# Kernel optimization log

Measured on AMD Instinct MI355X. Metric: run time of the kernel, lower is better.

Reference implementation:

```python
import jax, jax.numpy as jnp
import numpy as np

N = 50000        # nodes
E = 800000       # edges
R = 8            # relations
G = 64           # g_dim
H1 = 64          # h1_dim
H2 = 32          # h2_dim (per-head for transformer, output for sage)
HEADS = 4
EPS = 1e-5       # BatchNorm eps


def setup_inputs() -> dict:
    key = jax.random.key(0)
    ks = jax.random.split(key, 16)
    def rn(k, shape, scale=0.05):
        return jax.random.normal(k, shape, dtype=jnp.float32) * scale
    return {
        "node_features": jax.random.normal(ks[0], (N, G), dtype=jnp.float32),
        "node_type": jax.random.randint(ks[1], (N,), 0, 3),
        "edge_index": jax.random.randint(ks[2], (2, E), 0, N),
        "edge_type": jax.random.randint(ks[3], (E,), 0, R),
        # RGCNConv params (per-relation weight + root weight + bias)
        "rgcn_w": rn(ks[4], (R, G, H1)),
        "rgcn_root": rn(ks[5], (G, H1)),
        "rgcn_bias": jnp.zeros((H1,), jnp.float32),
        "bn1_g": jnp.ones((H1,), jnp.float32),
        "bn1_b": jnp.zeros((H1,), jnp.float32),
        # TransformerConv params (q/k/v projections + skip)
        "wq": rn(ks[6], (H1, HEADS * H2)), "bq": jnp.zeros((HEADS * H2,), jnp.float32),
        "wk": rn(ks[7], (H1, HEADS * H2)), "bk": jnp.zeros((HEADS * H2,), jnp.float32),
        "wv": rn(ks[8], (H1, HEADS * H2)), "bv": jnp.zeros((HEADS * H2,), jnp.float32),
        "wskip": rn(ks[9], (H1, HEADS * H2)), "bskip": jnp.zeros((HEADS * H2,), jnp.float32),
        "bn2_g": jnp.ones((HEADS * H2,), jnp.float32),
        "bn2_b": jnp.zeros((HEADS * H2,), jnp.float32),
        # SAGEConv params (lin_l on aggregated neighbors has bias; lin_r on root has none)
        "sage_wl": rn(ks[10], (HEADS * H2, H2)), "sage_bl": jnp.zeros((H2,), jnp.float32),
        "sage_wr": rn(ks[11], (HEADS * H2, H2)),
        "bn3_g": jnp.ones((H2,), jnp.float32),
        "bn3_b": jnp.zeros((H2,), jnp.float32),
    }


def _bn(x, g, b):
    # BatchNorm1d in training mode: biased batch statistics over nodes
    m = x.mean(0)
    v = x.var(0)
    return g * (x - m) * jax.lax.rsqrt(v + EPS) + b


def _match(res, d):
    # F.pad(res, (0, d - c)): pads with zeros if d > c, truncates if d < c
    c = res.shape[1]
    if d > c:
        return jnp.pad(res, ((0, 0), (0, d - c)))
    return res[:, :d]


def _forward(node_features, rgcn_w, rgcn_root, rgcn_bias, bn1_g, bn1_b,
             wq, bq, wk, bk, wv, bv, wskip, bskip, bn2_g, bn2_b,
             sage_wl, sage_bl, sage_wr, bn3_g, bn3_b,
             edge_index, edge_type):
    src, dst = edge_index[0], edge_index[1]
    x = node_features
    residual = x

    # ---- RGCNConv: per-relation transform, per-relation mean aggregation, sum over relations ----
    xr = jnp.einsum('nf,rfh->nrh', x, rgcn_w)            # [N,R,H1]
    msg = xr[src, edge_type]                              # [E,H1]
    seg = dst * R + edge_type                             # segment per (node, relation)
    sums = jax.ops.segment_sum(msg, seg, num_segments=N * R)
    cnt = jax.ops.segment_sum(jnp.ones((E,), msg.dtype), seg, num_segments=N * R)
    agg = (sums / jnp.maximum(cnt, 1.0)[:, None]).reshape(N, R, H1).sum(1)
    h = agg + x @ rgcn_root + rgcn_bias
    h = jax.nn.leaky_relu(_bn(h, bn1_g, bn1_b))
    x = h + _match(residual, h.shape[1])
    residual = x

    # ---- TransformerConv: edge softmax attention, concat heads, + skip projection ----
    q = (x @ wq + bq).reshape(N, HEADS, H2)
    k = (x @ wk + bk).reshape(N, HEADS, H2)
    v = (x @ wv + bv).reshape(N, HEADS, H2)
    logits = (q[dst] * k[src]).sum(-1) / jnp.sqrt(jnp.float32(H2))  # [E,HEADS]
    mx = jax.ops.segment_max(logits, dst, num_segments=N)
    ex = jnp.exp(logits - mx[dst])
    den = jax.ops.segment_sum(ex, dst, num_segments=N)
    alpha = ex / jnp.maximum(den[dst], 1e-16)
    out = jax.ops.segment_sum(alpha[:, :, None] * v[src], dst, num_segments=N)
    h = out.reshape(N, HEADS * H2) + x @ wskip + bskip
    h = jax.nn.leaky_relu(_bn(h, bn2_g, bn2_b))
    x = h + _match(residual, h.shape[1])
    residual = x

    # ---- SAGEConv: mean neighbor aggregation + root transform ----
    nsum = jax.ops.segment_sum(x[src], dst, num_segments=N)
    ncnt = jax.ops.segment_sum(jnp.ones((E,), x.dtype), dst, num_segments=N)
    nmean = nsum / jnp.maximum(ncnt, 1.0)[:, None]
    h = nmean @ sage_wl + sage_bl + x @ sage_wr
    h = jax.nn.leaky_relu(_bn(h, bn3_g, bn3_b))
    return h + _match(residual, h.shape[1])


def reference(node_features, node_type, edge_index, edge_type,
              rgcn_w, rgcn_root, rgcn_bias, bn1_g, bn1_b,
              wq, bq, wk, bk, wv, bv, wskip, bskip, bn2_g, bn2_b,
              sage_wl, sage_bl, sage_wr, bn3_g, bn3_b):
    # node_type is unused by the original forward
    return _forward(node_features, rgcn_w, rgcn_root, rgcn_bias, bn1_g, bn1_b,
                    wq, bq, wk, bk, wv, bv, wskip, bskip, bn2_g, bn2_b,
                    sage_wl, sage_bl, sage_wr, bn3_g, bn3_b,
                    edge_index, edge_type)
```

## Files before the change

### kernel.cpp

```cpp
#include <hip/hip_runtime.h>
#include <stdint.h>

#define NN 50000
#define NE 800000
#define NR (NN*8)
#define SCAN_BS 512
#define NB2 782
#define INV_N (1.0f/50000.0f)
#define BN_EPS 1e-5f

typedef unsigned short ushort_t;
typedef unsigned char uchar_t;
typedef short bf16x8 __attribute__((ext_vector_type(8)));
typedef float f32x4 __attribute__((ext_vector_type(4)));
typedef float f32x2 __attribute__((ext_vector_type(2)));

__device__ __forceinline__ ushort_t f2bf(float f){
    unsigned int u = __float_as_uint(f);
    u += 0x7FFFu + ((u >> 16) & 1u);
    return (ushort_t)(u >> 16);
}
__device__ __forceinline__ float bf2f(ushort_t h){ return __uint_as_float(((unsigned int)h) << 16); }
__device__ __forceinline__ float bflo(unsigned int u){ return __uint_as_float(u << 16); }
__device__ __forceinline__ float bfhi(unsigned int u){ return __uint_as_float(u & 0xFFFF0000u); }

__device__ __forceinline__ unsigned int f4_to_fp8(float a, float b, float c, float d){
    int v = __builtin_amdgcn_cvt_pk_fp8_f32(a, b, 0, false);
    v = __builtin_amdgcn_cvt_pk_fp8_f32(c, d, v, true);
    return (unsigned int)v;
}
__device__ __forceinline__ void fp8_to_f4(unsigned int u, float& a, float& b, float& c, float& d){
    f32x2 lo = __builtin_amdgcn_cvt_pk_f32_fp8(u, false);
    f32x2 hi = __builtin_amdgcn_cvt_pk_f32_fp8(u, true);
    a = lo.x; b = lo.y; c = hi.x; d = hi.y;
}

__global__ void k_prep(const float* __restrict__ nf,
                       const float* __restrict__ rgcn_w, const float* __restrict__ root,
                       const float* __restrict__ wq, const float* __restrict__ wk,
                       const float* __restrict__ wv, const float* __restrict__ wsk,
                       const float* __restrict__ bq, const float* __restrict__ bk,
                       const float* __restrict__ bv, const float* __restrict__ bsk,
                       const float* __restrict__ wl, const float* __restrict__ wr,
                       const int* __restrict__ ei, const int* __restrict__ et,
                       int* __restrict__ deg, uint2* __restrict__ sr,
                       ushort_t* __restrict__ xb, uchar_t* __restrict__ xb8,
                       ushort_t* __restrict__ Wcat,
                       ushort_t* __restrict__ Wt2, float* __restrict__ bcat,
                       ushort_t* __restrict__ Wsage){
    int i = blockIdx.x*256 + threadIdx.x;
    const int NXB = NN*16;
    if (i < NXB){
        float4 v = ((const float4*)nf)[i];
        ushort4 h;
        h.x = f2bf(v.x); h.y = f2bf(v.y); h.z = f2bf(v.z); h.w = f2bf(v.w);
        ((ushort4*)xb)[i] = h;
        ((unsigned int*)xb8)[i] = f4_to_fp8(v.x, v.y, v.z, v.w);
        return;
    }
    int j = i - NXB;
    if (j < 64*576){
        int h = j / 576, k = j - h*576;
        float v = (k < 512) ? rgcn_w[(size_t)k*64 + h] : root[(size_t)(k-512)*64 + h];
        Wcat[j] = f2bf(v);
    } else if (j < 64*576 + 512*64){
        int jj = j - 64*576;
        int c = jj >> 6, k = jj & 63;
        int mt = c >> 7, cc = c & 127;
        const float* W = (mt==0)?wq:(mt==1)?wk:(mt==2)?wv:wsk;
        Wt2[jj] = f2bf(W[(size_t)k*128 + cc]);
    } else if (j < 64*576 + 512*64 + 512){
        int c = j - (64*576 + 512*64);
        int mt = c >> 7, cc = c & 127;
        const float* B = (mt==0)?bq:(mt==1)?bk:(mt==2)?bv:bsk;
        bcat[c] = B[cc];
    } else if (j < 64*576 + 512*64 + 512 + 32*256){
        int jj = j - (64*576 + 512*64 + 512);
        int c = jj >> 8, k = jj & 255;
        float v = (k < 128) ? wr[(size_t)k*32 + c] : wl[(size_t)(k-128)*32 + c];
        Wsage[jj] = f2bf(v);
    } else {
        int e = j - (64*576 + 512*64 + 512 + 32*256);
        if (e < NE){
            int seg = ei[NE + e]*8 + et[e];
            int rank = atomicAdd(&deg[seg], 1);
            uint2 o; o.x = (unsigned)seg; o.y = (unsigned)rank;
            sr[e] = o;
        }
    }
}

__global__ void k_scan1(const int* __restrict__ deg, int* __restrict__ tmp, int* __restrict__ bsum){
    __shared__ int s[SCAN_BS];
    int t = threadIdx.x;
    int i = blockIdx.x*SCAN_BS + t;
    s[t] = (i < NR) ? deg[i] : 0;
    __syncthreads();
    for (int off = 1; off < SCAN_BS; off <<= 1){
        int add = (t >= off) ? s[t-off] : 0;
        __syncthreads();
        s[t] += add;
        __syncthreads();
    }
    if (i < NR) tmp[i] = s[t];
    if (t == SCAN_BS-1) bsum[blockIdx.x] = s[t];
}

__global__ void k_scan2(int* __restrict__ bsum){
    __shared__ int s[1024];
    int t = threadIdx.x;
    s[t] = (t < NB2) ? bsum[t] : 0;
    __syncthreads();
    for (int off = 1; off < 1024; off <<= 1){
        int v = (t >= off) ? s[t-off] : 0;
        __syncthreads();
        s[t] += v;
        __syncthreads();
    }
    if (t < NB2) bsum[t] = s[t];
}

__global__ void k_scan3(const int* __restrict__ tmp, const int* __restrict__ bsum, int* __restrict__ rs){
    int i = blockIdx.x*256 + threadIdx.x;
    if (i < NR){
        int b = i >> 9;
        int off = (b > 0) ? bsum[b-1] : 0;
        rs[i+1] = tmp[i] + off;
        if (i == 0) rs[0] = 0;
    }
}

__global__ void k_fill(const int* __restrict__ ei, const uint2* __restrict__ sr,
                       const int* __restrict__ rs, int* __restrict__ csr){
    int e = blockIdx.x*256 + threadIdx.x;
    if (e < NE){
        uint2 s = sr[e];
        csr[rs[s.x] + (int)s.y] = ei[e];
    }
}

__global__ __launch_bounds__(256) void rgcn_fused(const ushort_t* __restrict__ xb,
                                                  const uchar_t* __restrict__ xb8,
                                                  const int* __restrict__ rs,
                                                  const int* __restrict__ csr,
                                                  const ushort_t* __restrict__ Wcat,
                                                  const float* __restrict__ bias,
                                                  float* __restrict__ h1pre){
    __shared__ ushort_t Ml[16*520];
    int w = threadIdx.x >> 6, lane = threadIdx.x & 63;
    int quad = lane >> 4, l4 = lane & 15;
    int row0 = blockIdx.x * 16;
    int n0 = row0 + w*4;
    int rsel = (lane < 9 ? lane : 8);
    int rb = rs[n0*8 + rsel];
    int eb0 = __shfl(rb, 0);
    int dg0 = __shfl(rb, 8) - eb0;
    int idx = (lane < dg0) ? csr[eb0 + lane] : 0;
    for (int j = 0; j < 4; ++j){
        int lrow = (w*4 + j)*520;
        int ebase = __shfl(rb, 0);
        int enext = __shfl(rb, 8);
        int rb_next = 0, idxn = 0;
        if (j < 3){
            rb_next = rs[(n0 + j + 1)*8 + rsel];
            idxn = csr[min(enext + lane, NE - 1)];
        }
        int e0a = __shfl(rb, quad),     e1a = __shfl(rb, quad + 1);
        int e0b = __shfl(rb, quad + 4), e1b = __shfl(rb, quad + 5);
        int oa = e0a - ebase, la = e1a - e0a;
        int ob = e0b - ebase, lb = e1b - e0b;
        int laf = min(la, max(64 - oa, 0));
        int lbf = min(lb, max(64 - ob, 0));
        int ml = max(laf, lbf);
        ml = max(ml, __shfl_xor(ml, 16));
        ml = max(ml, __shfl_xor(ml, 32));
        f32x2 aA0 = {0.f,0.f}, aA1 = {0.f,0.f};
        f32x2 aB0 = {0.f,0.f}, aB1 = {0.f,0.f};
        for (int i = 0; i < ml; i += 4){
            unsigned int uA[4], uB[4];
#pragma unroll
            for (int u = 0; u < 4; ++u){
                int jA = oa + i + u, jB = ob + i + u;
                int tA = __shfl(idx, jA & 63);
                int tB = __shfl(idx, jB & 63);
                tA = ((i + u) < laf) ? tA : 0;
                tB = ((i + u) < lbf) ? tB : 0;
                uA[u] = *(const unsigned int*)(xb8 + (size_t)tA*64 + l4*4);
                uB[u] = *(const unsigned int*)(xb8 + (size_t)tB*64 + l4*4);
            }
#pragma unroll
            for (int u = 0; u < 4; ++u){
                unsigned int a = ((i + u) < laf) ? uA[u] : 0u;
                unsigned int b = ((i + u) < lbf) ? uB[u] : 0u;
                aA0 += __builtin_amdgcn_cvt_pk_f32_fp8(a, false);
                aA1 += __builtin_amdgcn_cvt_pk_f32_fp8(a, true);
                aB0 += __builtin_amdgcn_cvt_pk_f32_fp8(b, false);
                aB1 += __builtin_amdgcn_cvt_pk_f32_fp8(b, true);
            }
        }
        for (int i = laf; i < la; ++i){
            int t = csr[e0a + i];
            unsigned int a = *(const unsigned int*)(xb8 + (size_t)t*64 + l4*4);
            aA0 += __builtin_amdgcn_cvt_pk_f32_fp8(a, false);
            aA1 += __builtin_amdgcn_cvt_pk_f32_fp8(a, true);
        }
        for (int i = lbf; i < lb; ++i){
            int t = csr[e0b + i];
            unsigned int b = *(const unsigned int*)(xb8 + (size_t)t*64 + l4*4);
            aB0 += __builtin_amdgcn_cvt_pk_f32_fp8(b, false);
            aB1 += __builtin_amdgcn_cvt_pk_f32_fp8(b, true);
        }
        float inva = 1.f / fmaxf((float)la, 1.f);
        float invb = 1.f / fmaxf((float)lb, 1.f);
        ushort4 oA, oB;
        oA.x = f2bf(aA0.x*inva); oA.y = f2bf(aA0.y*inva); oA.z = f2bf(aA1.x*inva); oA.w = f2bf(aA1.y*inva);
        oB.x = f2bf(aB0.x*invb); oB.y = f2bf(aB0.y*invb); oB.z = f2bf(aB1.x*invb); oB.w = f2bf(aB1.y*invb);
        *(ushort4*)&Ml[lrow + quad*64 + l4*4] = oA;
        *(ushort4*)&Ml[lrow + (quad + 4)*64 + l4*4] = oB;
        if (j < 3){
            rb = rb_next;
            int ebn = __shfl(rb, 0);
            int dgn = __shfl(rb, 8) - ebn;
            idx = (lane < dgn) ? idxn : 0;
        }
    }
    __syncthreads();
    int m = l4;
    f32x4 acc = {};
#pragma unroll
    for (int kt = 0; kt < 18; ++kt){
        int kk = kt*32 + quad*8;
        bf16x8 a;
        if (kt < 16) a = *(const bf16x8*)&Ml[m*520 + kk];
        else         a = *(const bf16x8*)(xb + (size_t)(row0 + m)*64 + (kk - 512));
        bf16x8 b = *(const bf16x8*)(Wcat + (size_t)(w*16 + m)*576 + kk);
        acc = __builtin_amdgcn_mfma_f32_16x16x32_bf16(a, b, acc, 0, 0, 0);
    }
    int col = w*16 + m;
    float bz = bias[col];
#pragma unroll
    for (int i = 0; i < 4; ++i){
        int rr = row0 + quad*4 + i;
        h1pre[(size_t)rr*64 + col] = acc[i] + bz;
    }
}

#define QS 132
#define BS 68
__global__ __launch_bounds__(256) void gemm_qkvs(const float* __restrict__ h1pre,
                                                 const float* __restrict__ nf,
                                                 const float* __restrict__ s1, const float* __restrict__ q1,
                                                 const float* __restrict__ g1, const float* __restrict__ b1,
                                                 const ushort_t* __restrict__ Wt2,
                                                 const float* __restrict__ bcat,
                                                 ushort_t* __restrict__ qb,
                                                 uchar_t* __restrict__ kb8,
                                                 uchar_t* __restrict__ vb8,
                                                 ushort_t* __restrict__ sb){
    __shared__ ushort_t Bs[256*BS];
    __shared__ ushort_t pl[4][16*QS];
    int w = threadIdx.x >> 6, lane = threadIdx.x & 63;
    int m = lane & 15, quad = lane >> 4;
    int r0 = blockIdx.x*64 + w*16;
    int cg = blockIdx.y;
    int row = r0 + m;
    {
        int t = threadIdx.x;
        const ushort_t* wsrc = Wt2 + (size_t)cg*256*64;
#pragma unroll
        for (int u0 = 0; u0 < 8; ++u0){
            int u = u0*256 + t;
            int r = u >> 3, c8 = (u & 7)*8;
            *(uint4*)&Bs[r*BS + c8] = *(const uint4*)(wsrc + u*8);
        }
    }
    bf16x8 afrag[2];
#pragma unroll
    for (int kt = 0; kt < 2; ++kt){
        int db = kt*32 + quad*8;
        bf16x8 f = (bf16x8){0,0,0,0,0,0,0,0};
        if (row < NN){
            float4 h0 = *(const float4*)(h1pre + (size_t)row*64 + db);
            float4 h1 = *(const float4*)(h1pre + (size_t)row*64 + db + 4);
            float4 n0 = *(const float4*)(nf + (size_t)row*64 + db);
            float4 n1 = *(const float4*)(nf + (size_t)row*64 + db + 4);
            float4 sa = *(const float4*)(s1 + db);
            float4 sb_ = *(const float4*)(s1 + db + 4);
            float4 qa = *(const float4*)(q1 + db);
            float4 qb_ = *(const float4*)(q1 + db + 4);
            float4 ga = *(const float4*)(g1 + db);
            float4 gb_ = *(const float4*)(g1 + db + 4);
            float4 ba = *(const float4*)(b1 + db);
            float4 bb_ = *(const float4*)(b1 + db + 4);
            float hh[8] = {h0.x,h0.y,h0.z,h0.w,h1.x,h1.y,h1.z,h1.w};
            float nn[8] = {n0.x,n0.y,n0.z,n0.w,n1.x,n1.y,n1.z,n1.w};
            float SS[8] = {sa.x,sa.y,sa.z,sa.w,sb_.x,sb_.y,sb_.z,sb_.w};
            float QQ[8] = {qa.x,qa.y,qa.z,qa.w,qb_.x,qb_.y,qb_.z,qb_.w};
            float GG[8] = {ga.x,ga.y,ga.z,ga.w,gb_.x,gb_.y,gb_.z,gb_.w};
            float BB[8] = {ba.x,ba.y,ba.z,ba.w,bb_.x,bb_.y,bb_.z,bb_.w};
#pragma unroll
            for (int e = 0; e < 8; ++e){
                float mm = SS[e] * INV_N;
                float vv = QQ[e] * INV_N - mm*mm;
                float A = rsqrtf(fmaxf(vv, 0.f) + BN_EPS) * GG[e];
                float C = BB[e] - mm * A;
                float y = fmaf(hh[e], A, C);
                y = (y >= 0.f) ? y : 0.01f*y;
                f[e] = (short)f2bf(y + nn[e]);
            }
        }
        afrag[kt] = f;
    }
    __syncthreads();
    f32x4 acc[16] = {};
#pragma unroll
    for (int kt = 0; kt < 2; ++kt){
        int kk = kt*32 + quad*8;
#pragma unroll
        for (int ct = 0; ct < 16; ++ct){
            bf16x8 b = *(const bf16x8*)&Bs[(size_t)(ct*16 + m)*BS + kk];
            acc[ct] = __builtin_amdgcn_mfma_f32_16x16x32_bf16(afrag[kt], b, acc[ct], 0, 0, 0);
        }
    }
#pragma unroll
    for (int ct = 0; ct < 8; ++ct){
        int g = cg*256 + ct*16 + m;
        float bz = bcat[g];
        int cc = g & 127;
#pragma unroll
        for (int i = 0; i < 4; ++i)
            pl[w][(quad*4 + i)*QS + cc] = f2bf(acc[ct][i] + bz);
    }
    if (cg == 0){
#pragma unroll
        for (int t = 0; t < 4; ++t){
            int u = t*64 + lane;
            int r = u >> 4, c = (u & 15)*8;
            int gr = r0 + r;
            if (gr < NN) *(uint4*)(qb + (size_t)gr*128 + c) = *(const uint4*)&pl[w][r*QS + c];
        }
    } else {
#pragma unroll
        for (int t = 0; t < 4; ++t){
            int u = t*64 + lane;
            int r = u >> 4, c = (u & 15)*8;
            int gr = r0 + r;
            if (gr < NN){
                uint4 vv4 = *(const uint4*)&pl[w][r*QS + c];
                uint2 o;
                o.x = f4_to_fp8(bflo(vv4.x), bfhi(vv4.x), bflo(vv4.y), bfhi(vv4.y));
                o.y = f4_to_fp8(bflo(vv4.z), bfhi(vv4.z), bflo(vv4.w), bfhi(vv4.w));
                *(uint2*)(vb8 + (size_t)gr*128 + c) = o;
            }
        }
    }
#pragma unroll
    for (int ct = 8; ct < 16; ++ct){
        int g = cg*256 + ct*16 + m;
        float bz = bcat[g];
        int cc = g & 127;
#pragma unroll
        for (int i = 0; i < 4; ++i)
            pl[w][(quad*4 + i)*QS + cc] = f2bf(acc[ct][i] + bz);
    }
    if (cg == 0){
#pragma unroll
        for (int t = 0; t < 4; ++t){
            int u = t*64 + lane;
            int r = u >> 4, c = (u & 15)*8;
            int gr = r0 + r;
            if (gr < NN){
                uint4 kk4 = *(const uint4*)&pl[w][r*QS + c];
                uint2 o;
                o.x = f4_to_fp8(bflo(kk4.x), bfhi(kk4.x), bflo(kk4.y), bfhi(kk4.y));
                o.y = f4_to_fp8(bflo(kk4.z), bfhi(kk4.z), bflo(kk4.w), bfhi(kk4.w));
                *(uint2*)(kb8 + (size_t)gr*128 + c) = o;
            }
        }
    } else {
#pragma unroll
        for (int t = 0; t < 4; ++t){
            int u = t*64 + lane;
            int r = u >> 4, c = (u & 15)*8;
            int gr = r0 + r;
            if (gr < NN) *(uint4*)(sb + (size_t)gr*128 + c) = *(const uint4*)&pl[w][r*QS + c];
        }
    }
}

__global__ __launch_bounds__(256) void sage_gemm(const ushort_t* __restrict__ x2b,
                                                 const ushort_t* __restrict__ nmeanb,
                                                 const ushort_t* __restrict__ Wsage,
                                                 const float* __restrict__ bl,
                                                 float* __restrict__ h3){
    int wv = threadIdx.x >> 6, lane = threadIdx.x & 63;
    int r0 = blockIdx.x*64 + wv*16;
    int m = lane & 15, quad = lane >> 4;
    int row = r0 + m;
    f32x4 acc[2] = {};
#pragma unroll
    for (int kt = 0; kt < 8; ++kt){
        int kk = kt*32 + quad*8;
        bf16x8 a;
        if (row < NN){
            const ushort_t* ap = (kt < 4) ? (x2b + (size_t)row*128 + kk)
                                          : (nmeanb + (size_t)row*128 + (kk - 128));
            a = *(const bf16x8*)ap;
        } else {
            a = (bf16x8){0,0,0,0,0,0,0,0};
        }
#pragma unroll
        for (int ct = 0; ct < 2; ++ct){
            bf16x8 b = *(const bf16x8*)(Wsage + (size_t)(ct*16 + m)*256 + kk);
            acc[ct] = __builtin_amdgcn_mfma_f32_16x16x32_bf16(a, b, acc[ct], 0, 0, 0);
        }
    }
#pragma unroll
    for (int ct = 0; ct < 2; ++ct){
        int col = ct*16 + m;
        float bz = bl[col];
#pragma unroll
        for (int i = 0; i < 4; ++i){
            int rr = r0 + quad*4 + i;
            if (rr < NN) h3[(size_t)rr*32 + col] = acc[ct][i] + bz;
        }
    }
}

template<int C>
__global__ __launch_bounds__(256) void bn_stats(const float* __restrict__ X, int ld,
                                                float* __restrict__ sums, float* __restrict__ sumsq){
    __shared__ float s1[256], s2[256];
    int t = threadIdx.x;
    int c = t & (C-1);
    const int rpb = 256 / C;
    int r = blockIdx.x * rpb + (t / C);
    int rstride = gridDim.x * rpb;
    float a = 0.f, b = 0.f;
    for (; r < NN; r += rstride){
        float v = X[(size_t)r*ld + c];
        a += v; b += v*v;
    }
    s1[t] = a; s2[t] = b;
    __syncthreads();
    for (int off = 128; off >= C; off >>= 1){
        if (t < off){ s1[t] += s1[t+off]; s2[t] += s2[t+off]; }
        __syncthreads();
    }
    if (t < C){ atomicAdd(&sums[t], s1[t]); atomicAdd(&sumsq[t], s2[t]); }
}

__device__ __forceinline__ float bn_leaky(float z, float m, float rsv, float g, float b){
    float y = (z - m) * rsv * g + b;
    return y >= 0.f ? y : 0.01f * y;
}

__global__ void bn_apply2(const float* __restrict__ h2, const float* __restrict__ h1pre,
                          const float* __restrict__ nf,
                          const float* __restrict__ g1, const float* __restrict__ b1,
                          const float* __restrict__ s1, const float* __restrict__ q1,
                          const float* __restrict__ g2, const float* __restrict__ b2,
                          const float* __restrict__ s2, const float* __restrict__ q2,
                          float* __restrict__ x2r, ushort_t* __restrict__ x2b,
                          uchar_t* __restrict__ x28){
    int i = blockIdx.x*256 + threadIdx.x;
    if (i >= NN*128) return;
    int n = i >> 7, c = i & 127;
    float m2 = s2[c] * INV_N;
    float v2 = q2[c] * INV_N - m2*m2;
    float rsv2 = rsqrtf(fmaxf(v2, 0.f) + BN_EPS);
    float val = bn_leaky(h2[i], m2, rsv2, g2[c], b2[c]);
    if (c < 64){
        float m1 = s1[c] * INV_N;
        float v1 = q1[c] * INV_N - m1*m1;
        float rsv1 = rsqrtf(fmaxf(v1, 0.f) + BN_EPS);
        val += bn_leaky(h1pre[(size_t)n*64 + c], m1, rsv1, g1[c], b1[c]) + nf[(size_t)n*64 + c];
    }
    if (c < 32) x2r[(size_t)n*32 + c] = val;
    x2b[i] = f2bf(val);
    int p = __builtin_amdgcn_cvt_pk_fp8_f32(val, val, 0, false);
    x28[i] = (uchar_t)(p & 0xFF);
}

__global__ void bn_apply3(const float* __restrict__ h3, const float* __restrict__ x2r,
                          const float* __restrict__ g, const float* __restrict__ b,
                          const float* __restrict__ sums, const float* __restrict__ sumsq,
                          float* __restrict__ out){
    int i = blockIdx.x*256 + threadIdx.x;
    if (i >= NN*32) return;
    int c = i & 31;
    float m = sums[c] * INV_N;
    float v = sumsq[c] * INV_N - m*m;
    float rsv = rsqrtf(fmaxf(v, 0.f) + BN_EPS);
    out[i] = bn_leaky(h3[i], m, rsv, g[c], b[c]) + x2r[i];
}

__global__ __launch_bounds__(256) void attn_kernel(const ushort_t* __restrict__ qb,
                                                   const uchar_t* __restrict__ kb8,
                                                   const uchar_t* __restrict__ vb8,
                                                   const ushort_t* __restrict__ sb,
                                                   const int* __restrict__ rs,
                                                   const int* __restrict__ csr,
                                                   float* __restrict__ h2){
    int w = threadIdx.x >> 6, lane = threadIdx.x & 63;
    int n = blockIdx.x*4 + w;
    if (n >= NN) return;
    int half = lane >> 5, l5 = lane & 31;
    int e0 = rs[n*8], e1 = rs[n*8 + 8];
    int deg = e1 - e0;
    uint2 qu = *(const uint2*)(qb + (size_t)n*128 + l5*4);
    uint2 sbv = *(const uint2*)(sb + (size_t)n*128 + l5*4);
    float q0 = bflo(qu.x), q1 = bfhi(qu.x), q2 = bflo(qu.y), q3 = bfhi(qu.y);
    const float scale = 0.17677669529663687f;
    int idx = 0;
    if (lane < deg) idx = csr[e0 + lane];
    int dcap = min(deg, 64);
    int nt = (dcap + 7) >> 3;
    float den = 0.f, a0 = 0.f, a1 = 0.f, a2 = 0.f, a3 = 0.f;
    for (int t = 0; t < nt; ++t){
        int i2 = t*8 + half*4;
        int j0 = i2, j1 = i2+1, j2 = i2+2, j3 = i2+3;
        bool v0 = j0 < dcap, v1 = j1 < dcap, v2 = j2 < dcap, v3 = j3 < dcap;
        int s0 = __shfl(idx, j0 & 63); s0 = v0 ? s0 : 0;
        int s1 = __shfl(idx, j1 & 63); s1 = v1 ? s1 : 0;
        int s2 = __shfl(idx, j2 & 63); s2 = v2 ? s2 : 0;
        int s3 = __shfl(idx, j3 & 63); s3 = v3 ? s3 : 0;
        unsigned int ku0 = *(const unsigned int*)(kb8 + (size_t)s0*128 + l5*4);
        unsigned int ku1 = *(const unsigned int*)(kb8 + (size_t)s1*128 + l5*4);
        unsigned int ku2 = *(const unsigned int*)(kb8 + (size_t)s2*128 + l5*4);
        unsigned int ku3 = *(const unsigned int*)(kb8 + (size_t)s3*128 + l5*4);
        unsigned int vu0 = *(const unsigned int*)(vb8 + (size_t)s0*128 + l5*4);
        unsigned int vu1 = *(const unsigned int*)(vb8 + (size_t)s1*128 + l5*4);
        unsigned int vu2 = *(const unsigned int*)(vb8 + (size_t)s2*128 + l5*4);
        unsigned int vu3 = *(const unsigned int*)(vb8 + (size_t)s3*128 + l5*4);
        float ka, kb_, kc, kd;
        fp8_to_f4(ku0, ka, kb_, kc, kd);
        float p0 = q0*ka + q1*kb_ + q2*kc + q3*kd;
        fp8_to_f4(ku1, ka, kb_, kc, kd);
        float p1 = q0*ka + q1*kb_ + q2*kc + q3*kd;
        fp8_to_f4(ku2, ka, kb_, kc, kd);
        float p2 = q0*ka + q1*kb_ + q2*kc + q3*kd;
        fp8_to_f4(ku3, ka, kb_, kc, kd);
        float p3 = q0*ka + q1*kb_ + q2*kc + q3*kd;
        p0 += __shfl_xor(p0, 1); p1 += __shfl_xor(p1, 1); p2 += __shfl_xor(p2, 1); p3 += __shfl_xor(p3, 1);
        p0 += __shfl_xor(p0, 2); p1 += __shfl_xor(p1, 2); p2 += __shfl_xor(p2, 2); p3 += __shfl_xor(p3, 2);
        p0 += __shfl_xor(p0, 4); p1 += __shfl_xor(p1, 4); p2 += __shfl_xor(p2, 4); p3 += __shfl_xor(p3, 4);
        float w0 = v0 ? __expf(p0 * scale) : 0.f;
        float w1 = v1 ? __expf(p1 * scale) : 0.f;
        float w2 = v2 ? __expf(p2 * scale) : 0.f;
        float w3 = v3 ? __expf(p3 * scale) : 0.f;
        den += w0 + w1 + w2 + w3;
        float va, vb_, vc, vd;
        fp8_to_f4(vu0, va, vb_, vc, vd);
        a0 = fmaf(w0, va, a0); a1 = fmaf(w0, vb_, a1); a2 = fmaf(w0, vc, a2); a3 = fmaf(w0, vd, a3);
        fp8_to_f4(vu1, va, vb_, vc, vd);
        a0 = fmaf(w1, va, a0); a1 = fmaf(w1, vb_, a1); a2 = fmaf(w1, vc, a2); a3 = fmaf(w1, vd, a3);
        fp8_to_f4(vu2, va, vb_, vc, vd);
        a0 = fmaf(w2, va, a0); a1 = fmaf(w2, vb_, a1); a2 = fmaf(w2, vc, a2); a3 = fmaf(w2, vd, a3);
        fp8_to_f4(vu3, va, vb_, vc, vd);
        a0 = fmaf(w3, va, a0); a1 = fmaf(w3, vb_, a1); a2 = fmaf(w3, vc, a2); a3 = fmaf(w3, vd, a3);
    }
    for (int e = 64 + half; e < deg; e += 2){
        int s = csr[e0 + e];
        unsigned int ku = *(const unsigned int*)(kb8 + (size_t)s*128 + l5*4);
        unsigned int vu = *(const unsigned int*)(vb8 + (size_t)s*128 + l5*4);
        float ka, kb_, kc, kd;
        fp8_to_f4(ku, ka, kb_, kc, kd);
        float p = q0*ka + q1*kb_ + q2*kc + q3*kd;
        p += __shfl_xor(p, 1);
        p += __shfl_xor(p, 2);
        p += __shfl_xor(p, 4);
        float wg = __expf(p * scale);
        den += wg;
        float va, vb_, vc, vd;
        fp8_to_f4(vu, va, vb_, vc, vd);
        a0 = fmaf(wg, va, a0); a1 = fmaf(wg, vb_, a1); a2 = fmaf(wg, vc, a2); a3 = fmaf(wg, vd, a3);
    }
    den += __shfl_xor(den, 32);
    a0 += __shfl_xor(a0, 32); a1 += __shfl_xor(a1, 32);
    a2 += __shfl_xor(a2, 32); a3 += __shfl_xor(a3, 32);
    if (half == 0){
        float inv = (den > 0.f) ? 1.f/den : 0.f;
        float4 o;
        o.x = bflo(sbv.x) + a0*inv;
        o.y = bfhi(sbv.x) + a1*inv;
        o.z = bflo(sbv.y) + a2*inv;
        o.w = bfhi(sbv.y) + a3*inv;
        *(float4*)(h2 + (size_t)n*128 + l5*4) = o;
    }
}

__global__ __launch_bounds__(256) void sage_agg(const uchar_t* __restrict__ x28,
                                                const int* __restrict__ rs,
                                                const int* __restrict__ csr,
                                                ushort_t* __restrict__ nmeanb){
    int w = threadIdx.x >> 6, lane = threadIdx.x & 63;
    int n = blockIdx.x*4 + w;
    if (n >= NN) return;
    int half = lane >> 5, l5 = lane & 31;
    int e0 = rs[n*8], e1 = rs[n*8 + 8];
    int deg = e1 - e0;
    int idx = 0;
    if (lane < deg) idx = csr[e0 + lane];
    int dcap = min(deg, 64);
    int nt = (dcap + 7) >> 3;
    f32x2 A0 = {0.f,0.f}, A1 = {0.f,0.f};
    for (int t = 0; t < nt; ++t){
        int i2 = t*8 + half*4;
        int j0 = i2, j1 = i2+1, j2 = i2+2, j3 = i2+3;
        bool v0 = j0 < dcap, v1 = j1 < dcap, v2 = j2 < dcap, v3 = j3 < dcap;
        int s0 = __shfl(idx, j0 & 63); s0 = v0 ? s0 : 0;
        int s1 = __shfl(idx, j1 & 63); s1 = v1 ? s1 : 0;
        int s2 = __shfl(idx, j2 & 63); s2 = v2 ? s2 : 0;
        int s3 = __shfl(idx, j3 & 63); s3 = v3 ? s3 : 0;
        unsigned int u0 = *(const unsigned int*)(x28 + (size_t)s0*128 + l5*4);
        unsigned int u1 = *(const unsigned int*)(x28 + (size_t)s1*128 + l5*4);
        unsigned int u2 = *(const unsigned int*)(x28 + (size_t)s2*128 + l5*4);
        unsigned int u3 = *(const unsigned int*)(x28 + (size_t)s3*128 + l5*4);
        u0 = v0 ? u0 : 0u; u1 = v1 ? u1 : 0u;
        u2 = v2 ? u2 : 0u; u3 = v3 ? u3 : 0u;
        A0 += __builtin_amdgcn_cvt_pk_f32_fp8(u0, false);
        A1 += __builtin_amdgcn_cvt_pk_f32_fp8(u0, true);
        A0 += __builtin_amdgcn_cvt_pk_f32_fp8(u1, false);
        A1 += __builtin_amdgcn_cvt_pk_f32_fp8(u1, true);
        A0 += __builtin_amdgcn_cvt_pk_f32_fp8(u2, false);
        A1 += __builtin_amdgcn_cvt_pk_f32_fp8(u2, true);
        A0 += __builtin_amdgcn_cvt_pk_f32_fp8(u3, false);
        A1 += __builtin_amdgcn_cvt_pk_f32_fp8(u3, true);
    }
    for (int e = 64 + half; e < deg; e += 2){
        int s = csr[e0 + e];
        unsigned int u = *(const unsigned int*)(x28 + (size_t)s*128 + l5*4);
        A0 += __builtin_amdgcn_cvt_pk_f32_fp8(u, false);
        A1 += __builtin_amdgcn_cvt_pk_f32_fp8(u, true);
    }
    float a0 = A0.x, a1 = A0.y, a2 = A1.x, a3 = A1.y;
    a0 += __shfl_xor(a0, 32); a1 += __shfl_xor(a1, 32);
    a2 += __shfl_xor(a2, 32); a3 += __shfl_xor(a3, 32);
    if (half == 0){
        float inv = 1.f / fmaxf((float)deg, 1.f);
        ushort4 o;
        o.x = f2bf(a0*inv); o.y = f2bf(a1*inv); o.z = f2bf(a2*inv); o.w = f2bf(a3*inv);
        *(ushort4*)(nmeanb + (size_t)n*128 + l5*4) = o;
    }
}

extern "C" void kernel_launch(void* const* d_in, const int* in_sizes, int n_in,
                              void* d_out, int out_size, void* d_ws, size_t ws_size,
                              hipStream_t stream){
    const float* nf      = (const float*)d_in[0];
    const int*   ei      = (const int*)d_in[2];
    const int*   et      = (const int*)d_in[3];
    const float* rgcn_w  = (const float*)d_in[4];
    const float* root    = (const float*)d_in[5];
    const float* rbias   = (const float*)d_in[6];
    const float* bn1g    = (const float*)d_in[7];
    const float* bn1b    = (const float*)d_in[8];
    const float* wq      = (const float*)d_in[9];
    const float* bq      = (const float*)d_in[10];
    const float* wk      = (const float*)d_in[11];
    const float* bk      = (const float*)d_in[12];
    const float* wv      = (const float*)d_in[13];
    const float* bv      = (const float*)d_in[14];
    const float* wsk     = (const float*)d_in[15];
    const float* bsk     = (const float*)d_in[16];
    const float* bn2g    = (const float*)d_in[17];
    const float* bn2b    = (const float*)d_in[18];
    const float* wl      = (const float*)d_in[19];
    const float* bl      = (const float*)d_in[20];
    const float* wr      = (const float*)d_in[21];
    const float* bn3g    = (const float*)d_in[22];
    const float* bn3b    = (const float*)d_in[23];
    float* out = (float*)d_out;

    char* base = (char*)d_ws;
    size_t off = 0;
    auto take = [&](size_t bytes) -> char* {
        char* p = base + off;
        off += (bytes + 255) & ~(size_t)255;
        return p;
    };
    int*      deg    = (int*)take((size_t)NR*4);
    float*    bns    = (float*)take(1024*4);
    char*     zend   = base + off;
    int*      rs     = (int*)take((size_t)(NR+1)*4);
    int*      tmp    = (int*)take((size_t)NR*4);
    int*      bsum   = (int*)take(1024*4);
    uint2*    sr     = (uint2*)take((size_t)NE*8);
    int*      csr    = (int*)take((size_t)NE*4);
    ushort_t* Wcat   = (ushort_t*)take(64*576*2);
    ushort_t* Wt2    = (ushort_t*)take(512*64*2);
    float*    bcat   = (float*)take(512*4);
    ushort_t* Wsage  = (ushort_t*)take(32*256*2);
    ushort_t* xb     = (ushort_t*)take((size_t)NN*64*2);
    uchar_t*  xb8    = (uchar_t*)take((size_t)NN*64);
    float*    h1pre  = (float*)take((size_t)NN*64*4);
    float*    h2     = (float*)take((size_t)NN*128*4);
    float*    x2r    = (float*)take((size_t)NN*32*4);
    ushort_t* sb     = (ushort_t*)take((size_t)NN*128*2);
    char*     bigA   = take((size_t)NN*512*2);
    if (off > ws_size) return;

    ushort_t* qb     = (ushort_t*)(bigA + (size_t)NN*128);
    uchar_t*  vb8    = (uchar_t*)(bigA + (size_t)NN*384);
    uchar_t*  kb8    = (uchar_t*)(bigA + (size_t)NN*640);
    ushort_t* x2b    = (ushort_t*)bigA;
    uchar_t*  x28    = (uchar_t*)(bigA + (size_t)NN*256);
    ushort_t* nmeanb = (ushort_t*)(bigA + (size_t)NN*512);
    float*    h3     = (float*)(bigA + (size_t)NN*768);

    hipMemsetAsync(deg, 0, (size_t)(zend - (char*)deg), stream);

    const int PREP_N = NN*16 + 64*576 + 512*64 + 512 + 32*256 + NE;
    k_prep <<<(PREP_N+255)/256, 256, 0, stream>>>(nf, rgcn_w, root, wq, wk, wv, wsk,
                                                  bq, bk, bv, bsk, wl, wr,
                                                  ei, et, deg, sr,
                                                  xb, xb8, Wcat, Wt2, bcat, Wsage);
    k_scan1<<<NB2, SCAN_BS, 0, stream>>>(deg, tmp, bsum);
    k_scan2<<<1, 1024, 0, stream>>>(bsum);
    k_scan3<<<(NR+255)/256, 256, 0, stream>>>(tmp, bsum, rs);
    k_fill <<<(NE+255)/256, 256, 0, stream>>>(ei, sr, rs, csr);

    const int NB4 = (NN + 3) / 4;
    const int NBG = (NN + 63) / 64;

    rgcn_fused<<<NN/16, 256, 0, stream>>>(xb, xb8, rs, csr, Wcat, rbias, h1pre);
    bn_stats<64><<<256, 256, 0, stream>>>(h1pre, 64, bns + 0, bns + 64);

    gemm_qkvs<<<dim3(NBG, 2), 256, 0, stream>>>(h1pre, nf, bns + 0, bns + 64, bn1g, bn1b,
                                                Wt2, bcat, qb, kb8, vb8, sb);
    attn_kernel<<<NB4, 256, 0, stream>>>(qb, kb8, vb8, sb, rs, csr, h2);
    bn_stats<128><<<256, 256, 0, stream>>>(h2, 128, bns + 128, bns + 256);
    bn_apply2<<<(NN*128+255)/256, 256, 0, stream>>>(h2, h1pre, nf,
                                                    bn1g, bn1b, bns + 0, bns + 64,
                                                    bn2g, bn2b, bns + 128, bns + 256,
                                                    x2r, x2b, x28);

    sage_agg<<<NB4, 256, 0, stream>>>(x28, rs, csr, nmeanb);
    sage_gemm<<<NBG, 256, 0, stream>>>(x2b, nmeanb, Wsage, bl, h3);
    bn_stats<32><<<256, 256, 0, stream>>>(h3, 32, bns + 384, bns + 416);
    bn_apply3<<<(NN*32+255)/256, 256, 0, stream>>>(h3, x2r, bn3g, bn3b, bns + 384, bns + 416, out);
}
```

Baseline: 401.7 us.

## Fuse BatchNorm statistics into producer kernels and merge QKV column groups

```diff
diff --git a/kernel.cpp b/kernel.cpp
--- a/kernel.cpp
+++ b/kernel.cpp
@@ -145,7 +145,8 @@
                                                   const int* __restrict__ csr,
                                                   const ushort_t* __restrict__ Wcat,
                                                   const float* __restrict__ bias,
-                                                  float* __restrict__ h1pre){
+                                                  float* __restrict__ h1pre,
+                                                  float* __restrict__ bns){
     __shared__ ushort_t Ml[16*520];
     int w = threadIdx.x >> 6, lane = threadIdx.x & 63;
     int quad = lane >> 4, l4 = lane & 15;
@@ -238,10 +239,19 @@
     }
     int col = w*16 + m;
     float bz = bias[col];
+    float s = 0.f, q = 0.f;
 #pragma unroll
     for (int i = 0; i < 4; ++i){
         int rr = row0 + quad*4 + i;
-        h1pre[(size_t)rr*64 + col] = acc[i] + bz;
+        float y = acc[i] + bz;
+        h1pre[(size_t)rr*64 + col] = y;
+        s += y; q += y*y;
+    }
+    s += __shfl_xor(s, 16); q += __shfl_xor(q, 16);
+    s += __shfl_xor(s, 32); q += __shfl_xor(q, 32);
+    if (quad == 0){
+        atomicAdd(&bns[col], s);
+        atomicAdd(&bns[64 + col], q);
     }
 }
 
@@ -262,18 +272,7 @@
     int w = threadIdx.x >> 6, lane = threadIdx.x & 63;
     int m = lane & 15, quad = lane >> 4;
     int r0 = blockIdx.x*64 + w*16;
-    int cg = blockIdx.y;
     int row = r0 + m;
-    {
-        int t = threadIdx.x;
-        const ushort_t* wsrc = Wt2 + (size_t)cg*256*64;
-#pragma unroll
-        for (int u0 = 0; u0 < 8; ++u0){
-            int u = u0*256 + t;
-            int r = u >> 3, c8 = (u & 7)*8;
-            *(uint4*)&Bs[r*BS + c8] = *(const uint4*)(wsrc + u*8);
-        }
-    }
     bf16x8 afrag[2];
 #pragma unroll
     for (int kt = 0; kt < 2; ++kt){
@@ -311,79 +310,92 @@
         }
         afrag[kt] = f;
     }
-    __syncthreads();
-    f32x4 acc[16] = {};
-#pragma unroll
-    for (int kt = 0; kt < 2; ++kt){
-        int kk = kt*32 + quad*8;
-#pragma unroll
-        for (int ct = 0; ct < 16; ++ct){
-            bf16x8 b = *(const bf16x8*)&Bs[(size_t)(ct*16 + m)*BS + kk];
-            acc[ct] = __builtin_amdgcn_mfma_f32_16x16x32_bf16(afrag[kt], b, acc[ct], 0, 0, 0);
-        }
-    }
-#pragma unroll
-    for (int ct = 0; ct < 8; ++ct){
-        int g = cg*256 + ct*16 + m;
-        float bz = bcat[g];
-        int cc = g & 127;
-#pragma unroll
-        for (int i = 0; i < 4; ++i)
-            pl[w][(quad*4 + i)*QS + cc] = f2bf(acc[ct][i] + bz);
-    }
-    if (cg == 0){
-#pragma unroll
-        for (int t = 0; t < 4; ++t){
-            int u = t*64 + lane;
-            int r = u >> 4, c = (u & 15)*8;
-            int gr = r0 + r;
-            if (gr < NN) *(uint4*)(qb + (size_t)gr*128 + c) = *(const uint4*)&pl[w][r*QS + c];
-        }
-    } else {
-#pragma unroll
-        for (int t = 0; t < 4; ++t){
-            int u = t*64 + lane;
-            int r = u >> 4, c = (u & 15)*8;
-            int gr = r0 + r;
-            if (gr < NN){
-                uint4 vv4 = *(const uint4*)&pl[w][r*QS + c];
-                uint2 o;
-                o.x = f4_to_fp8(bflo(vv4.x), bfhi(vv4.x), bflo(vv4.y), bfhi(vv4.y));
-                o.y = f4_to_fp8(bflo(vv4.z), bfhi(vv4.z), bflo(vv4.w), bfhi(vv4.w));
-                *(uint2*)(vb8 + (size_t)gr*128 + c) = o;
-            }
-        }
-    }
-#pragma unroll
-    for (int ct = 8; ct < 16; ++ct){
-        int g = cg*256 + ct*16 + m;
-        float bz = bcat[g];
-        int cc = g & 127;
-#pragma unroll
-        for (int i = 0; i < 4; ++i)
-            pl[w][(quad*4 + i)*QS + cc] = f2bf(acc[ct][i] + bz);
-    }
-    if (cg == 0){
-#pragma unroll
-        for (int t = 0; t < 4; ++t){
-            int u = t*64 + lane;
-            int r = u >> 4, c = (u & 15)*8;
-            int gr = r0 + r;
-            if (gr < NN){
-                uint4 kk4 = *(const uint4*)&pl[w][r*QS + c];
-                uint2 o;
-                o.x = f4_to_fp8(bflo(kk4.x), bfhi(kk4.x), bflo(kk4.y), bfhi(kk4.y));
-                o.y = f4_to_fp8(bflo(kk4.z), bfhi(kk4.z), bflo(kk4.w), bfhi(kk4.w));
-                *(uint2*)(kb8 + (size_t)gr*128 + c) = o;
-            }
-        }
-    } else {
-#pragma unroll
-        for (int t = 0; t < 4; ++t){
-            int u = t*64 + lane;
-            int r = u >> 4, c = (u & 15)*8;
-            int gr = r0 + r;
-            if (gr < NN) *(uint4*)(sb + (size_t)gr*128 + c) = *(const uint4*)&pl[w][r*QS + c];
+    for (int cg = 0; cg < 2; ++cg){
+        __syncthreads();
+        {
+            int t = threadIdx.x;
+            const ushort_t* wsrc = Wt2 + (size_t)cg*256*64;
+#pragma unroll
+            for (int u0 = 0; u0 < 8; ++u0){
+                int u = u0*256 + t;
+                int r = u >> 3, c8 = (u & 7)*8;
+                *(uint4*)&Bs[r*BS + c8] = *(const uint4*)(wsrc + u*8);
+            }
+        }
+        __syncthreads();
+        f32x4 acc[16] = {};
+#pragma unroll
+        for (int kt = 0; kt < 2; ++kt){
+            int kk = kt*32 + quad*8;
+#pragma unroll
+            for (int ct = 0; ct < 16; ++ct){
+                bf16x8 b = *(const bf16x8*)&Bs[(size_t)(ct*16 + m)*BS + kk];
+                acc[ct] = __builtin_amdgcn_mfma_f32_16x16x32_bf16(afrag[kt], b, acc[ct], 0, 0, 0);
+            }
+        }
+#pragma unroll
+        for (int ct = 0; ct < 8; ++ct){
+            int g = cg*256 + ct*16 + m;
+            float bz = bcat[g];
+            int cc = g & 127;
+#pragma unroll
+            for (int i = 0; i < 4; ++i)
+                pl[w][(quad*4 + i)*QS + cc] = f2bf(acc[ct][i] + bz);
+        }
+        if (cg == 0){
+#pragma unroll
+            for (int t = 0; t < 4; ++t){
+                int u = t*64 + lane;
+                int r = u >> 4, c = (u & 15)*8;
+                int gr = r0 + r;
+                if (gr < NN) *(uint4*)(qb + (size_t)gr*128 + c) = *(const uint4*)&pl[w][r*QS + c];
+            }
+        } else {
+#pragma unroll
+            for (int t = 0; t < 4; ++t){
+                int u = t*64 + lane;
+                int r = u >> 4, c = (u & 15)*8;
+                int gr = r0 + r;
+                if (gr < NN){
+                    uint4 vv4 = *(const uint4*)&pl[w][r*QS + c];
+                    uint2 o;
+                    o.x = f4_to_fp8(bflo(vv4.x), bfhi(vv4.x), bflo(vv4.y), bfhi(vv4.y));
+                    o.y = f4_to_fp8(bflo(vv4.z), bfhi(vv4.z), bflo(vv4.w), bfhi(vv4.w));
+                    *(uint2*)(vb8 + (size_t)gr*128 + c) = o;
+                }
+            }
+        }
+#pragma unroll
+        for (int ct = 8; ct < 16; ++ct){
+            int g = cg*256 + ct*16 + m;
+            float bz = bcat[g];
+            int cc = g & 127;
+#pragma unroll
+            for (int i = 0; i < 4; ++i)
+                pl[w][(quad*4 + i)*QS + cc] = f2bf(acc[ct][i] + bz);
+        }
+        if (cg == 0){
+#pragma unroll
+            for (int t = 0; t < 4; ++t){
+                int u = t*64 + lane;
+                int r = u >> 4, c = (u & 15)*8;
+                int gr = r0 + r;
+                if (gr < NN){
+                    uint4 kk4 = *(const uint4*)&pl[w][r*QS + c];
+                    uint2 o;
+                    o.x = f4_to_fp8(bflo(kk4.x), bfhi(kk4.x), bflo(kk4.y), bfhi(kk4.y));
+                    o.y = f4_to_fp8(bflo(kk4.z), bfhi(kk4.z), bflo(kk4.w), bfhi(kk4.w));
+                    *(uint2*)(kb8 + (size_t)gr*128 + c) = o;
+                }
+            }
+        } else {
+#pragma unroll
+            for (int t = 0; t < 4; ++t){
+                int u = t*64 + lane;
+                int r = u >> 4, c = (u & 15)*8;
+                int gr = r0 + r;
+                if (gr < NN) *(uint4*)(sb + (size_t)gr*128 + c) = *(const uint4*)&pl[w][r*QS + c];
+            }
         }
     }
 }
@@ -392,7 +404,8 @@
                                                  const ushort_t* __restrict__ nmeanb,
                                                  const ushort_t* __restrict__ Wsage,
                                                  const float* __restrict__ bl,
-                                                 float* __restrict__ h3){
+                                                 float* __restrict__ h3,
+                                                 float* __restrict__ bns3){
     int wv = threadIdx.x >> 6, lane = threadIdx.x & 63;
     int r0 = blockIdx.x*64 + wv*16;
     int m = lane & 15, quad = lane >> 4;
@@ -415,6 +428,7 @@
             acc[ct] = __builtin_amdgcn_mfma_f32_16x16x32_bf16(a, b, acc[ct], 0, 0, 0);
         }
     }
+    float s[2] = {0.f, 0.f}, q[2] = {0.f, 0.f};
 #pragma unroll
     for (int ct = 0; ct < 2; ++ct){
         int col = ct*16 + m;
@@ -422,32 +436,26 @@
 #pragma unroll
         for (int i = 0; i < 4; ++i){
             int rr = r0 + quad*4 + i;
-            if (rr < NN) h3[(size_t)rr*32 + col] = acc[ct][i] + bz;
-        }
-    }
-}
-
-template<int C>
-__global__ __launch_bounds__(256) void bn_stats(const float* __restrict__ X, int ld,
-                                                float* __restrict__ sums, float* __restrict__ sumsq){
-    __shared__ float s1[256], s2[256];
-    int t = threadIdx.x;
-    int c = t & (C-1);
-    const int rpb = 256 / C;
-    int r = blockIdx.x * rpb + (t / C);
-    int rstride = gridDim.x * rpb;
-    float a = 0.f, b = 0.f;
-    for (; r < NN; r += rstride){
-        float v = X[(size_t)r*ld + c];
-        a += v; b += v*v;
-    }
-    s1[t] = a; s2[t] = b;
-    __syncthreads();
-    for (int off = 128; off >= C; off >>= 1){
-        if (t < off){ s1[t] += s1[t+off]; s2[t] += s2[t+off]; }
-        __syncthreads();
-    }
-    if (t < C){ atomicAdd(&sums[t], s1[t]); atomicAdd(&sumsq[t], s2[t]); }
+            if (rr < NN){
+                float y = acc[ct][i] + bz;
+                h3[(size_t)rr*32 + col] = y;
+                s[ct] += y; q[ct] += y*y;
+            }
+        }
+    }
+#pragma unroll
+    for (int ct = 0; ct < 2; ++ct){
+        s[ct] += __shfl_xor(s[ct], 16); q[ct] += __shfl_xor(q[ct], 16);
+        s[ct] += __shfl_xor(s[ct], 32); q[ct] += __shfl_xor(q[ct], 32);
+    }
+    if (quad == 0){
+#pragma unroll
+        for (int ct = 0; ct < 2; ++ct){
+            int col = ct*16 + m;
+            atomicAdd(&bns3[col], s[ct]);
+            atomicAdd(&bns3[32 + col], q[ct]);
+        }
+    }
 }
 
 __device__ __forceinline__ float bn_leaky(float z, float m, float rsv, float g, float b){
@@ -501,10 +509,11 @@
                                                    const ushort_t* __restrict__ sb,
                                                    const int* __restrict__ rs,
                                                    const int* __restrict__ csr,
-                                                   float* __restrict__ h2){
+                                                   float* __restrict__ h2,
+                                                   float* __restrict__ bns2){
+    __shared__ float sm[2][4][128];
     int w = threadIdx.x >> 6, lane = threadIdx.x & 63;
     int n = blockIdx.x*4 + w;
-    if (n >= NN) return;
     int half = lane >> 5, l5 = lane & 31;
     int e0 = rs[n*8], e1 = rs[n*8 + 8];
     int deg = e1 - e0;
@@ -579,14 +588,26 @@
     den += __shfl_xor(den, 32);
     a0 += __shfl_xor(a0, 32); a1 += __shfl_xor(a1, 32);
     a2 += __shfl_xor(a2, 32); a3 += __shfl_xor(a3, 32);
+    float inv = (den > 0.f) ? 1.f/den : 0.f;
+    float o0 = bflo(sbv.x) + a0*inv;
+    float o1 = bfhi(sbv.x) + a1*inv;
+    float o2 = bflo(sbv.y) + a2*inv;
+    float o3 = bfhi(sbv.y) + a3*inv;
     if (half == 0){
-        float inv = (den > 0.f) ? 1.f/den : 0.f;
-        float4 o;
-        o.x = bflo(sbv.x) + a0*inv;
-        o.y = bfhi(sbv.x) + a1*inv;
-        o.z = bflo(sbv.y) + a2*inv;
-        o.w = bfhi(sbv.y) + a3*inv;
+        float4 o; o.x = o0; o.y = o1; o.z = o2; o.w = o3;
         *(float4*)(h2 + (size_t)n*128 + l5*4) = o;
+        float4 t; t.x = o0; t.y = o1; t.z = o2; t.w = o3;
+        *(float4*)&sm[0][w][l5*4] = t;
+    } else {
+        float4 t; t.x = o0*o0; t.y = o1*o1; t.z = o2*o2; t.w = o3*o3;
+        *(float4*)&sm[1][w][l5*4] = t;
+    }
+    __syncthreads();
+    {
+        int t = threadIdx.x;
+        int st = t >> 7, c = t & 127;
+        float v = sm[st][0][c] + sm[st][1][c] + sm[st][2][c] + sm[st][3][c];
+        atomicAdd(&bns2[st*128 + c], v);
     }
 }
 
@@ -724,20 +745,17 @@
     const int NB4 = (NN + 3) / 4;
     const int NBG = (NN + 63) / 64;
 
-    rgcn_fused<<<NN/16, 256, 0, stream>>>(xb, xb8, rs, csr, Wcat, rbias, h1pre);
-    bn_stats<64><<<256, 256, 0, stream>>>(h1pre, 64, bns + 0, bns + 64);
-
-    gemm_qkvs<<<dim3(NBG, 2), 256, 0, stream>>>(h1pre, nf, bns + 0, bns + 64, bn1g, bn1b,
-                                                Wt2, bcat, qb, kb8, vb8, sb);
-    attn_kernel<<<NB4, 256, 0, stream>>>(qb, kb8, vb8, sb, rs, csr, h2);
-    bn_stats<128><<<256, 256, 0, stream>>>(h2, 128, bns + 128, bns + 256);
+    rgcn_fused<<<NN/16, 256, 0, stream>>>(xb, xb8, rs, csr, Wcat, rbias, h1pre, bns);
+
+    gemm_qkvs<<<NBG, 256, 0, stream>>>(h1pre, nf, bns + 0, bns + 64, bn1g, bn1b,
+                                       Wt2, bcat, qb, kb8, vb8, sb);
+    attn_kernel<<<NB4, 256, 0, stream>>>(qb, kb8, vb8, sb, rs, csr, h2, bns + 128);
     bn_apply2<<<(NN*128+255)/256, 256, 0, stream>>>(h2, h1pre, nf,
                                                     bn1g, bn1b, bns + 0, bns + 64,
                                                     bn2g, bn2b, bns + 128, bns + 256,
                                                     x2r, x2b, x28);
 
     sage_agg<<<NB4, 256, 0, stream>>>(x28, rs, csr, nmeanb);
-    sage_gemm<<<NBG, 256, 0, stream>>>(x2b, nmeanb, Wsage, bl, h3);
-    bn_stats<32><<<256, 256, 0, stream>>>(h3, 32, bns + 384, bns + 416);
+    sage_gemm<<<NBG, 256, 0, stream>>>(x2b, nmeanb, Wsage, bl, h3, bns + 384);
     bn_apply3<<<(NN*32+255)/256, 256, 0, stream>>>(h3, x2r, bn3g, bn3b, bns + 384, bns + 416, out);
 }
```

Measured after the change: 733.5 us. +82.6%, slower.
